# Performance work log

Measured on AMD Instinct MI355X. Metric: run time of the kernel, lower is better.

Reference implementation:

```python
import jax, jax.numpy as jnp
import numpy as np

DIM_Z = 256
N_HEADS = 8
R = DIM_Z // N_HEADS  # ternary_rank / rope head_dim
SCALE = 1.0           # ternary_scaling
THETA = 10000.0


def _rope_cos_sin(S, dtype):
    # returns cos, sin of shape [1, 1, S, R] (broadcast over batch and heads)
    inv_freq = 1.0 / (THETA ** (jnp.arange(0, R, 2, dtype=jnp.float32) / R))
    freqs = jnp.arange(S, dtype=jnp.float32)[:, None] * inv_freq[None, :]  # [S, R/2]
    emb = jnp.concatenate([freqs, freqs], axis=-1)  # [S, R]
    return jnp.cos(emb).astype(dtype)[None, None], jnp.sin(emb).astype(dtype)[None, None]


def _rot_half(x):
    h = x.shape[-1] // 2
    return jnp.concatenate([-x[..., h:], x[..., :h]], axis=-1)


def _apply(x, cos, sin):
    return x * cos + _rot_half(x) * sin


def _apply_o(x, cos, sin):
    return x * cos - _rot_half(x) * sin


def _compute_F(qz, mask, u, v, cos, sin):
    # qz: [N, S, D]; u, v: [D, D]; mask: [N, 1, S, S] or None
    N, S, D = qz.shape
    qu = (qz @ u.T) * SCALE
    qv = (qz @ v.T) * SCALE
    qu = qu.reshape(N, S, N_HEADS, R).transpose(0, 2, 1, 3)  # [N, H, S, R]
    qv = qv.reshape(N, S, N_HEADS, R).transpose(0, 2, 1, 3)
    qu_rot = _apply(qu, cos, sin)
    qu_o = _apply_o(qu, cos, sin)
    qv_rot = _apply(qv, cos, sin)
    F_mat = jnp.einsum('nhsr,nhtr->nhst', qu_rot, qv_rot)  # [N, H, S, S]
    if mask is not None:
        F_mat = F_mat + mask
    return F_mat, qu_o, qv_rot


def _compute_G(qh, qu_o, qv_rot, u, v, cos, sin):
    # qh: [N, H, S, S]
    N, H, S, _ = qh.shape
    g1 = _apply_o(jnp.einsum('nhst,nhtr->nhsr', qh, qv_rot), cos, sin)
    g2 = _apply(jnp.einsum('nhts,nhtr->nhsr', qh, qu_o), cos, sin)
    g1 = g1.transpose(0, 2, 1, 3).reshape(N, S, H * R)
    g2 = g2.transpose(0, 2, 1, 3).reshape(N, S, H * R)
    return (g1 @ u + g2 @ v) * SCALE  # [N, S, D]


def setup_inputs() -> dict:
    key = jax.random.key(0)
    ks = jax.random.split(key, 8)
    B, C, P, D = 8, 32, 128, DIM_Z
    std = 0.2  # ternary_init_std
    return {
        'qz': jax.random.normal(ks[0], (B, C, P, D), jnp.float32),
        'dep_mask_time': jax.random.normal(ks[1], (B * C, 1, P, P), jnp.float32),
        'dep_mask_chan': jax.random.normal(ks[2], (B * P, 1, C, C), jnp.float32),
        'u_time': std * jax.random.normal(ks[3], (D, D), jnp.float32),
        'v_time': std * jax.random.normal(ks[4], (D, D), jnp.float32),
        'u_chan': std * jax.random.normal(ks[5], (D, D), jnp.float32),
        'v_chan': std * jax.random.normal(ks[6], (D, D), jnp.float32),
    }


def reference(qz, dep_mask_time, dep_mask_chan, u_time, v_time, u_chan, v_chan):
    B, C, P, D = qz.shape
    H = N_HEADS
    cos_t, sin_t = _rope_cos_sin(P, qz.dtype)
    cos_c, sin_c = _rope_cos_sin(C, qz.dtype)

    qz_t = qz.reshape(B * C, P, D)
    F_t, quo_t, qv_t = _compute_F(qz_t, dep_mask_time, u_time, v_time, cos_t, sin_t)
    qz_c = qz.transpose(0, 2, 1, 3).reshape(B * P, C, D)
    F_c, quo_c, qv_c = _compute_F(qz_c, dep_mask_chan, u_chan, v_chan, cos_c, sin_c)

    # Joint softmax over combined time+channel candidates: [B, H, C, P, P+C]
    F_t_r = F_t.reshape(B, C, H, P, P).transpose(0, 2, 1, 3, 4)
    F_c_r = F_c.reshape(B, P, H, C, C).transpose(0, 2, 3, 1, 4)
    logits = jnp.concatenate([F_t_r, F_c_r], axis=-1)
    # regularize_h = 1/dim_z -> logits / regularize_h == logits * D; softmax in fp32
    qh = jax.nn.softmax(logits.astype(jnp.float32) * D, axis=-1)
    qh_t = qh[..., :P].transpose(0, 2, 1, 3, 4).reshape(B * C, H, P, P).astype(qz.dtype)
    qh_c = qh[..., P:].transpose(0, 3, 1, 2, 4).reshape(B * P, H, C, C).astype(qz.dtype)

    m_time = _compute_G(qh_t, quo_t, qv_t, u_time, v_time, cos_t, sin_t).reshape(B, C, P, D)
    m_chan = _compute_G(qh_c, quo_c, qv_c, u_chan, v_chan, cos_c, sin_c)
    m_chan = m_chan.reshape(B, P, C, D).transpose(0, 2, 1, 3)
    return m_time, m_chan
```

## Files before the change

### kernel.cpp

```cpp
#include <hip/hip_runtime.h>
#include <hip/hip_bf16.h>
#include <math.h>

#define LOG2T_16 0.8304820237218406f

typedef __attribute__((ext_vector_type(8))) short short8;
typedef __attribute__((ext_vector_type(4))) float f32x4;

#define PERM_LO 0x05040100u
#define PERM_HI 0x07060302u

__device__ __forceinline__ float bf2f(unsigned short u) {
    union { float f; unsigned int i; } x; x.i = ((unsigned int)u) << 16; return x.f;
}
__device__ __forceinline__ unsigned short f2b(float f) {
    __hip_bfloat16 h = __float2bfloat16(f);
    union { __hip_bfloat16 h; unsigned short u; } x; x.h = h; return x.u;
}

__device__ __forceinline__ float v5_dot32(const float* qurow, const float* row) {
    float dot = 0.f;
#pragma unroll
    for (int q = 0; q < 8; q++) {
        float4 x = *(const float4*)(row + q * 4);
        dot = fmaf(qurow[q * 4 + 0], x.x, dot);
        dot = fmaf(qurow[q * 4 + 1], x.y, dot);
        dot = fmaf(qurow[q * 4 + 2], x.z, dot);
        dot = fmaf(qurow[q * 4 + 3], x.w, dot);
    }
    return dot;
}

__device__ __forceinline__ void v5_fma32(float p_, const float* row, float* acc) {
#pragma unroll
    for (int q = 0; q < 8; q++) {
        float4 x = *(const float4*)(row + q * 4);
        float xs[4] = {x.x, x.y, x.z, x.w};
#pragma unroll
        for (int i = 0; i < 4; i++)
            acc[q * 4 + i] = fmaf(p_, xs[i], acc[q * 4 + i]);
    }
}

__global__ __launch_bounds__(256) void v10_prepB(
    const float* __restrict__ u_t, const float* __restrict__ v_t,
    const float* __restrict__ u_c, const float* __restrict__ v_c,
    unsigned int* __restrict__ Bp, unsigned int* __restrict__ Pp)
{
    __shared__ float Ts[64][65];
    const int mtx = blockIdx.y;
    const float* src = (mtx == 0) ? u_t : (mtx == 1) ? v_t : (mtx == 2) ? u_c : v_c;
    unsigned int* dst  = Bp + (size_t)mtx * 65536;
    unsigned int* pdst = Pp + (size_t)mtx * 65536;
    const int k0 = (blockIdx.x >> 2) * 64;
    const int c0 = (blockIdx.x & 3) * 64;
    const int tid = threadIdx.x;
    const int lr = tid >> 2;
    const int lc0 = (tid & 3) * 16;
    float av[16];
#pragma unroll
    for (int q = 0; q < 4; q++) {
        float4 x = *(const float4*)(src + (size_t)(k0 + lr) * 256 + c0 + lc0 + q * 4);
        *(float4*)&av[q * 4] = x;
        *(float4*)&Ts[lr][lc0 + q * 4] = x;
    }
#pragma unroll
    for (int q = 0; q < 4; q++) {
        unsigned int w[4];
#pragma unroll
        for (int e = 0; e < 4; e++) {
            float x = av[q * 4 + e];
            unsigned short hi = f2b(x);
            unsigned short lo = f2b(x - bf2f(hi));
            w[e] = (unsigned int)hi | ((unsigned int)lo << 16);
        }
        *(uint4*)(pdst + (size_t)(k0 + lr) * 256 + c0 + lc0 + q * 4) =
            make_uint4(w[0], w[1], w[2], w[3]);
    }
    __syncthreads();
#pragma unroll
    for (int q = 0; q < 4; q++) {
        unsigned int w[4];
#pragma unroll
        for (int e = 0; e < 4; e++) {
            float x = Ts[lc0 + q * 4 + e][lr];
            unsigned short hi = f2b(x);
            unsigned short lo = f2b(x - bf2f(hi));
            w[e] = (unsigned int)hi | ((unsigned int)lo << 16);
        }
        *(uint4*)(dst + (size_t)(c0 + lr) * 256 + k0 + lc0 + q * 4) =
            make_uint4(w[0], w[1], w[2], w[3]);
    }
}

__global__ __launch_bounds__(256) void v10_proj(
    const float* __restrict__ qz,
    const unsigned int* __restrict__ Pu, const unsigned int* __restrict__ Pv,
    float* __restrict__ qu_rot, float* __restrict__ qv_rot, int chan, int posmask)
{
    __shared__ __align__(16) unsigned short Ah[128][40];
    __shared__ __align__(16) unsigned short Al[128][40];
    __shared__ __align__(16) unsigned short Bh[128][40];
    __shared__ __align__(16) unsigned short Bl[128][40];
    const int row0 = blockIdx.x * 128;
    const int col0 = blockIdx.y * 128;
    const unsigned int* Bsrc = (col0 < 256) ? Pu : Pv;
    float* Cout = (col0 < 256) ? qu_rot : qv_rot;
    const int ccol0 = col0 & 255;
    const int tid = threadIdx.x;
    const int sr = tid >> 1;
    const int sk = (tid & 1) * 16;
    const int wv = tid >> 6;
    const int lane = tid & 63;
    const int wr = (wv >> 1) * 64, wc = (wv & 1) * 64;
    const int fr = lane & 15;
    const int fk = (lane >> 4) * 8;

    int arow = row0 + sr;
    if (chan) {
        int b = arow >> 12, p = (arow >> 5) & 127, c = arow & 31;
        arow = (b * 32 + c) * 128 + p;
    }
    const float* aptr = qz + (size_t)arow * 256 + sk;
    const unsigned int* bptr = Bsrc + (size_t)(ccol0 + sr) * 256 + sk;

    f32x4 acc[4][4] = {};

    for (int k0 = 0; k0 < 256; k0 += 32) {
        float av[16];
#pragma unroll
        for (int q = 0; q < 4; q++)
            *(float4*)&av[q * 4] = *(const float4*)(aptr + k0 + q * 4);
        unsigned int wh[8], wl[8];
#pragma unroll
        for (int e = 0; e < 8; e++) {
            unsigned short h0 = f2b(av[2 * e]), h1 = f2b(av[2 * e + 1]);
            unsigned short l0 = f2b(av[2 * e] - bf2f(h0));
            unsigned short l1 = f2b(av[2 * e + 1] - bf2f(h1));
            wh[e] = (unsigned int)h0 | ((unsigned int)h1 << 16);
            wl[e] = (unsigned int)l0 | ((unsigned int)l1 << 16);
        }
        *(uint4*)&Ah[sr][sk]     = make_uint4(wh[0], wh[1], wh[2], wh[3]);
        *(uint4*)&Ah[sr][sk + 8] = make_uint4(wh[4], wh[5], wh[6], wh[7]);
        *(uint4*)&Al[sr][sk]     = make_uint4(wl[0], wl[1], wl[2], wl[3]);
        *(uint4*)&Al[sr][sk + 8] = make_uint4(wl[4], wl[5], wl[6], wl[7]);
#pragma unroll
        for (int q = 0; q < 4; q++) {
            uint4 w = *(const uint4*)(bptr + k0 + q * 4);
            *(uint2*)&Bh[sr][sk + q * 4] = make_uint2(
                __builtin_amdgcn_perm(w.y, w.x, PERM_LO),
                __builtin_amdgcn_perm(w.w, w.z, PERM_LO));
            *(uint2*)&Bl[sr][sk + q * 4] = make_uint2(
                __builtin_amdgcn_perm(w.y, w.x, PERM_HI),
                __builtin_amdgcn_perm(w.w, w.z, PERM_HI));
        }
        __syncthreads();
        short8 ah[4], al[4];
#pragma unroll
        for (int i = 0; i < 4; i++) {
            ah[i] = *(const short8*)&Ah[wr + i * 16 + fr][fk];
            al[i] = *(const short8*)&Al[wr + i * 16 + fr][fk];
        }
#pragma unroll
        for (int j = 0; j < 4; j++) {
            const int bc = wc + j * 16 + fr;
            short8 bh = *(const short8*)&Bh[bc][fk];
            short8 bl = *(const short8*)&Bl[bc][fk];
#pragma unroll
            for (int i = 0; i < 4; i++) {
                acc[i][j] = __builtin_amdgcn_mfma_f32_16x16x32_bf16(ah[i], bh, acc[i][j], 0, 0, 0);
                acc[i][j] = __builtin_amdgcn_mfma_f32_16x16x32_bf16(ah[i], bl, acc[i][j], 0, 0, 0);
                acc[i][j] = __builtin_amdgcn_mfma_f32_16x16x32_bf16(al[i], bh, acc[i][j], 0, 0, 0);
                acc[i][j] = __builtin_amdgcn_mfma_f32_16x16x32_bf16(al[i], bl, acc[i][j], 0, 0, 0);
            }
        }
        __syncthreads();
    }
    const float fscale = exp2f(-(float)fr * LOG2T_16);
#pragma unroll
    for (int i = 0; i < 4; i++) {
#pragma unroll
        for (int r = 0; r < 4; r++) {
            int mr = row0 + wr + i * 16 + (lane >> 4) * 4 + r;
            float pos = (float)(mr & posmask);
            float sn, cs;
            sincosf(pos * fscale, &sn, &cs);
            float* op = Cout + (size_t)mr * 256 + ccol0 + wc + fr;
#pragma unroll
            for (int t = 0; t < 2; t++) {
                float x = acc[i][2 * t][r], y = acc[i][2 * t + 1][r];
                op[t * 32]      = x * cs - y * sn;
                op[t * 32 + 16] = y * cs + x * sn;
            }
        }
    }
}

__global__ __launch_bounds__(256) void v5_stats_t(
    const float* __restrict__ quR, const float* __restrict__ qvR,
    const float* __restrict__ mask, float* __restrict__ omax, float* __restrict__ osum)
{
    __shared__ float Qv[128][36];
    const int bid = blockIdx.x;
    const int n = bid & 255, h = bid >> 8;
    const int b = n >> 5, c = n & 31;
    const int tid = threadIdx.x;
    for (int idx = tid * 4; idx < 4096; idx += 1024) {
        int s = idx >> 5, r = idx & 31;
        *(float4*)&Qv[s][r] = *(const float4*)(qvR + ((size_t)(n * 128 + s)) * 256 + h * 32 + r);
    }
    const int s = tid >> 1, toff = (tid & 1) * 64;
    float qurow[32];
    const float* qptr = quR + ((size_t)(n * 128 + s)) * 256 + h * 32;
#pragma unroll
    for (int q = 0; q < 8; q++) {
        float4 x = *(const float4*)(qptr + q * 4);
        qurow[q * 4 + 0] = x.x; qurow[q * 4 + 1] = x.y; qurow[q * 4 + 2] = x.z; qurow[q * 4 + 3] = x.w;
    }
    __syncthreads();
    const float* mrow = mask + (size_t)n * 16384 + s * 128 + toff;
    float mx = -1e30f, sm = 0.f;
#pragma unroll 4
    for (int t = 0; t < 64; t++) {
        float dot = v5_dot32(qurow, &Qv[toff + t][0]);
        float vv = 256.f * (dot + mrow[t]);
        float nm = fmaxf(mx, vv);
        sm = sm * __expf(mx - nm) + __expf(vv - nm);
        mx = nm;
    }
    float omx = __shfl_xor(mx, 1);
    float osm = __shfl_xor(sm, 1);
    float fm = fmaxf(mx, omx);
    float fs = sm * __expf(mx - fm) + osm * __expf(omx - fm);
    if ((tid & 1) == 0) {
        int idx = ((b * 8 + h) * 32 + c) * 128 + s;
        omax[idx] = fm; osum[idx] = fs;
    }
}

__global__ __launch_bounds__(256) void v5_stats_c(
    const float* __restrict__ quR, const float* __restrict__ qvR,
    const float* __restrict__ mask, float* __restrict__ omax, float* __restrict__ osum)
{
    __shared__ float Qv[32][260];
    const int m = blockIdx.x;
    const int b = m >> 7, p = m & 127;
    const int tid = threadIdx.x;
    for (int idx = tid * 4; idx < 8192; idx += 1024) {
        int sc = idx >> 8, dd = idx & 255;
        *(float4*)&Qv[sc][dd] = *(const float4*)(qvR + ((size_t)m * 32 + sc) * 256 + dd);
    }
    const int h = tid >> 5, sc = tid & 31;
    float qurow[32];
    const float* qptr = quR + ((size_t)m * 32 + sc) * 256 + h * 32;
#pragma unroll
    for (int q = 0; q < 8; q++) {
        float4 x = *(const float4*)(qptr + q * 4);
        qurow[q * 4 + 0] = x.x; qurow[q * 4 + 1] = x.y; qurow[q * 4 + 2] = x.z; qurow[q * 4 + 3] = x.w;
    }
    __syncthreads();
    const float* mrow = mask + (size_t)m * 1024 + sc * 32;
    float mx = -1e30f, sm = 0.f;
#pragma unroll 4
    for (int t = 0; t < 32; t++) {
        float dot = v5_dot32(qurow, &Qv[t][h * 32]);
        float vv = 256.f * (dot + mrow[t]);
        float nm = fmaxf(mx, vv);
        sm = sm * __expf(mx - nm) + __expf(vv - nm);
        mx = nm;
    }
    int idx = ((b * 8 + h) * 32 + sc) * 128 + p;
    omax[idx] = mx; osum[idx] = sm;
}

__global__ __launch_bounds__(256) void v5_merge(
    const float* __restrict__ mt, const float* __restrict__ st,
    const float* __restrict__ mc, const float* __restrict__ sc,
    float* __restrict__ Mo, float* __restrict__ So)
{
    int i = blockIdx.x * 256 + threadIdx.x;
    float a = mt[i], b = mc[i];
    float mx = fmaxf(a, b);
    float s = st[i] * __expf(a - mx) + sc[i] * __expf(b - mx);
    Mo[i] = mx;
    So[i] = 1.f / s;
}

__global__ __launch_bounds__(256) void v8_G_t(
    const float* quR, const float* qvR,
    const float* __restrict__ mask, const float* __restrict__ Mr, const float* __restrict__ Sv,
    unsigned short* gpl)
{
    __shared__ __align__(16) unsigned short Pm[16384];
    __shared__ __align__(16) float Qv[128][36];
    unsigned short* QT = (unsigned short*)&Qv[0][0];
    const int bid = blockIdx.x;
    const int n = bid & 255, h = bid >> 8;
    const int b = n >> 5, c = n & 31;
    const int tid = threadIdx.x;
    const int lane = tid & 63, wv = tid >> 6;
    const int fr = lane & 15, kgl = lane >> 4;

    for (int idx = tid * 4; idx < 4096; idx += 1024) {
        int s = idx >> 5, r = idx & 31;
        *(float4*)&Qv[s][r] = *(const float4*)(qvR + ((size_t)(n * 128 + s)) * 256 + h * 32 + r);
    }
    {
        const int s = tid >> 1, toff = (tid & 1) * 64;
        float qurow[32];
        const float* qptr = quR + ((size_t)(n * 128 + s)) * 256 + h * 32;
#pragma unroll
        for (int q = 0; q < 8; q++) {
            float4 x = *(const float4*)(qptr + q * 4);
            qurow[q * 4 + 0] = x.x; qurow[q * 4 + 1] = x.y; qurow[q * 4 + 2] = x.z; qurow[q * 4 + 3] = x.w;
        }
        __syncthreads();
        const int rowidx = ((b * 8 + h) * 32 + c) * 128 + s;
        const float Mx = Mr[rowidx];
        const float Si = Sv[rowidx];
        const float* mrow = mask + (size_t)n * 16384 + s * 128 + toff;
#pragma unroll 4
        for (int t = 0; t < 64; t++) {
            float dot = v5_dot32(qurow, &Qv[toff + t][0]);
            float pv = __expf(256.f * (dot + mrow[t]) - Mx) * Si;
            int tg = toff + t;
            int ct = (((tg >> 3) ^ (s & 15)) << 3) | (tg & 7);
            Pm[s * 128 + ct] = f2b(pv);
        }
    }
    __syncthreads();
    {
        const int t = tid >> 1, rh = (tid & 1) * 16;
        const float* src = qvR + ((size_t)(n * 128 + t)) * 256 + h * 32 + rh;
        float v[16];
#pragma unroll
        for (int q = 0; q < 4; q++)
            *(float4*)&v[q * 4] = *(const float4*)(src + q * 4);
#pragma unroll
        for (int i = 0; i < 16; i++) {
            int r = rh + i;
            unsigned short hi = f2b(v[i]);
            unsigned short lo = f2b(v[i] - bf2f(hi));
            int ct = (((t >> 3) ^ (r & 15)) << 3) | (t & 7);
            QT[r * 128 + ct] = hi;
            QT[4096 + r * 128 + ct] = lo;
        }
    }
    __syncthreads();
    unsigned int g1h[8];
    {
        f32x4 acc[2][2] = {};
#pragma unroll
        for (int kw = 0; kw < 4; kw++) {
            short8 a[2];
#pragma unroll
            for (int i = 0; i < 2; i++) {
                int row = wv * 32 + i * 16 + fr;
                a[i] = *(const short8*)&Pm[row * 128 + (((kw * 4 + kgl) ^ (row & 15)) << 3)];
            }
            short8 bh[2], bl[2];
#pragma unroll
            for (int j = 0; j < 2; j++) {
                int r = j * 16 + fr;
                int off = r * 128 + (((kw * 4 + kgl) ^ (r & 15)) << 3);
                bh[j] = *(const short8*)&QT[off];
                bl[j] = *(const short8*)&QT[4096 + off];
            }
#pragma unroll
            for (int i = 0; i < 2; i++)
#pragma unroll
                for (int j = 0; j < 2; j++) {
                    acc[i][j] = __builtin_amdgcn_mfma_f32_16x16x32_bf16(a[i], bh[j], acc[i][j], 0, 0, 0);
                    acc[i][j] = __builtin_amdgcn_mfma_f32_16x16x32_bf16(a[i], bl[j], acc[i][j], 0, 0, 0);
                }
        }
#pragma unroll
        for (int i = 0; i < 2; i++)
#pragma unroll
            for (int reg = 0; reg < 4; reg++) {
                int s = wv * 32 + i * 16 + kgl * 4 + reg;
                float ang = (float)s * exp2f(-(float)fr * LOG2T_16);
                float sn, cs;
                __sincosf(ang, &sn, &cs);
                float x = acc[i][0][reg], y = acc[i][1][reg];
                g1h[i * 4 + reg] = (unsigned int)f2b(x * cs + y * sn)
                                 | ((unsigned int)f2b(y * cs - x * sn) << 16);
            }
    }
    __syncthreads();
    {
        const int t = tid >> 1, jh = (tid & 1) * 8;
        const float* base = quR + ((size_t)(n * 128 + t)) * 256 + h * 32;
        float aa[8], bb[8];
        *(float4*)&aa[0] = *(const float4*)(base + jh);
        *(float4*)&aa[4] = *(const float4*)(base + jh + 4);
        *(float4*)&bb[0] = *(const float4*)(base + jh + 16);
        *(float4*)&bb[4] = *(const float4*)(base + jh + 20);
#pragma unroll
        for (int i = 0; i < 8; i++) {
            int j = jh + i;
            float ang = 2.f * (float)t * exp2f(-(float)j * LOG2T_16);
            float s2, c2;
            __sincosf(ang, &s2, &c2);
            float o1 = aa[i] * c2 + bb[i] * s2;
            float o2 = bb[i] * c2 - aa[i] * s2;
            int ct1 = (((t >> 3) ^ (j & 15)) << 3) | (t & 7);
            unsigned short h1 = f2b(o1);
            QT[j * 128 + ct1] = h1;
            QT[4096 + j * 128 + ct1] = f2b(o1 - bf2f(h1));
            int r2 = j + 16;
            int ct2 = (((t >> 3) ^ (r2 & 15)) << 3) | (t & 7);
            unsigned short h2 = f2b(o2);
            QT[r2 * 128 + ct2] = h2;
            QT[4096 + r2 * 128 + ct2] = f2b(o2 - bf2f(h2));
        }
    }
    __syncthreads();
    unsigned int g2h[8];
    {
        f32x4 acc[2][2] = {};
#pragma unroll
        for (int kw = 0; kw < 4; kw++) {
            short8 ah[2], al[2];
#pragma unroll
            for (int i = 0; i < 2; i++) {
                int r = i * 16 + fr;
                int off = r * 128 + (((kw * 4 + kgl) ^ (r & 15)) << 3);
                ah[i] = *(const short8*)&QT[off];
                al[i] = *(const short8*)&QT[4096 + off];
            }
            short8 bfr[2];
#pragma unroll
            for (int jj = 0; jj < 2; jj++) {
                int scol = (2 * wv + jj) * 16 + fr;
#pragma unroll
                for (int j = 0; j < 8; j++) {
                    int t = kw * 32 + kgl * 8 + j;
                    int ct = (((scol >> 3) ^ (t & 15)) << 3) | (scol & 7);
                    bfr[jj][j] = (short)Pm[t * 128 + ct];
                }
            }
#pragma unroll
            for (int i = 0; i < 2; i++)
#pragma unroll
                for (int jj = 0; jj < 2; jj++) {
                    acc[i][jj] = __builtin_amdgcn_mfma_f32_16x16x32_bf16(ah[i], bfr[jj], acc[i][jj], 0, 0, 0);
                    acc[i][jj] = __builtin_amdgcn_mfma_f32_16x16x32_bf16(al[i], bfr[jj], acc[i][jj], 0, 0, 0);
                }
        }
#pragma unroll
        for (int jj = 0; jj < 2; jj++)
#pragma unroll
            for (int reg = 0; reg < 4; reg++) {
                int sv = (2 * wv + jj) * 16 + fr;
                int r = kgl * 4 + reg;
                float ang = (float)sv * exp2f(-(float)r * LOG2T_16);
                float sn, cs;
                __sincosf(ang, &sn, &cs);
                float x = acc[0][jj][reg], y = acc[1][jj][reg];
                g2h[jj * 4 + reg] = (unsigned int)f2b(x * cs - y * sn)
                                  | ((unsigned int)f2b(y * cs + x * sn) << 16);
            }
    }
    __syncthreads();
    {
#pragma unroll
        for (int i = 0; i < 2; i++)
#pragma unroll
            for (int reg = 0; reg < 4; reg++) {
                int s = wv * 32 + i * 16 + kgl * 4 + reg;
                unsigned int w = g1h[i * 4 + reg];
                Pm[s * 32 + fr] = (unsigned short)w;
                Pm[s * 32 + fr + 16] = (unsigned short)(w >> 16);
            }
#pragma unroll
        for (int jj = 0; jj < 2; jj++)
#pragma unroll
            for (int reg = 0; reg < 4; reg++) {
                int s = (2 * wv + jj) * 16 + fr;
                int r = kgl * 4 + reg;
                unsigned int w = g2h[jj * 4 + reg];
                Pm[4096 + s * 32 + r] = (unsigned short)w;
                Pm[4096 + s * 32 + r + 16] = (unsigned short)(w >> 16);
            }
    }
    __syncthreads();
    {
        const int s = tid >> 1, rh = (tid & 1) * 16;
        size_t baseu = ((size_t)(n * 128 + s)) * 512 + h * 64 + rh;
        *(uint4*)(gpl + baseu)      = *(const uint4*)&Pm[s * 32 + rh];
        *(uint4*)(gpl + baseu + 8)  = *(const uint4*)&Pm[s * 32 + rh + 8];
        *(uint4*)(gpl + baseu + 32) = *(const uint4*)&Pm[4096 + s * 32 + rh];
        *(uint4*)(gpl + baseu + 40) = *(const uint4*)&Pm[4096 + s * 32 + rh + 8];
    }
}

__global__ __launch_bounds__(256) void v8_G_c(
    const float* quR, const float* qvR,
    const float* __restrict__ mask, const float* __restrict__ Mr, const float* __restrict__ Sv,
    unsigned short* gpl)
{
    __shared__ float Qv[32][260];
    __shared__ unsigned short Pm[8][32][34];
    const int m = blockIdx.x;
    const int b = m >> 7, p = m & 127;
    const int tid = threadIdx.x;
    for (int idx = tid * 4; idx < 8192; idx += 1024) {
        int sc = idx >> 8, dd = idx & 255;
        *(float4*)&Qv[sc][dd] = *(const float4*)(qvR + ((size_t)m * 32 + sc) * 256 + dd);
    }
    const int h = tid >> 5, sc = tid & 31;
    {
        float qurow[32];
        const float* qptr = quR + ((size_t)m * 32 + sc) * 256 + h * 32;
#pragma unroll
        for (int q = 0; q < 8; q++) {
            float4 x = *(const float4*)(qptr + q * 4);
            qurow[q * 4 + 0] = x.x; qurow[q * 4 + 1] = x.y; qurow[q * 4 + 2] = x.z; qurow[q * 4 + 3] = x.w;
        }
        __syncthreads();
        const int rowidx = ((b * 8 + h) * 32 + sc) * 128 + p;
        const float Mx = Mr[rowidx], Si = Sv[rowidx];
        const float* mrow = mask + (size_t)m * 1024 + sc * 32;
#pragma unroll 4
        for (int t = 0; t < 32; t++) {
            float dot = v5_dot32(qurow, &Qv[t][h * 32]);
            float pv = __expf(256.f * (dot + mrow[t]) - Mx) * Si;
            Pm[h][t][sc] = f2b(pv);
        }
    }
    __syncthreads();
    float a[32] = {};
#pragma unroll 4
    for (int t = 0; t < 32; t++) {
        float p_ = bf2f(Pm[h][t][sc]);
        v5_fma32(p_, &Qv[t][h * 32], a);
    }
    float cs[16], sn[16];
#pragma unroll
    for (int i = 0; i < 16; i++) {
        float ang = (float)sc * exp2f(-(float)i * LOG2T_16);
        __sincosf(ang, &sn[i], &cs[i]);
    }
    unsigned int g1p[8], g1q[8];
#pragma unroll
    for (int j = 0; j < 8; j++) {
        int i0 = 2 * j, i1 = 2 * j + 1;
        float x0 = a[i0], y0 = a[16 + i0], x1 = a[i1], y1 = a[16 + i1];
        g1p[j] = (unsigned int)f2b(x0 * cs[i0] + y0 * sn[i0])
               | ((unsigned int)f2b(x1 * cs[i1] + y1 * sn[i1]) << 16);
        g1q[j] = (unsigned int)f2b(y0 * cs[i0] - x0 * sn[i0])
               | ((unsigned int)f2b(y1 * cs[i1] - x1 * sn[i1]) << 16);
    }
    __syncthreads();
    for (int idx = tid * 4; idx < 4096; idx += 1024) {
        int row = idx >> 7, rem = idx & 127;
        int h2 = rem >> 4, j0 = rem & 15;
        const float* base = quR + ((size_t)m * 32 + row) * 256 + h2 * 32;
        float4 a4 = *(const float4*)(base + j0);
        float4 b4 = *(const float4*)(base + j0 + 16);
        float aa[4] = {a4.x, a4.y, a4.z, a4.w};
        float bb[4] = {b4.x, b4.y, b4.z, b4.w};
        float o1[4], o2[4];
#pragma unroll
        for (int i = 0; i < 4; i++) {
            float ang = 2.f * (float)row * exp2f(-(float)(j0 + i) * LOG2T_16);
            float s2, c2;
            __sincosf(ang, &s2, &c2);
            o1[i] = aa[i] * c2 + bb[i] * s2;
            o2[i] = bb[i] * c2 - aa[i] * s2;
        }
        *(float4*)&Qv[row][h2 * 32 + j0]      = make_float4(o1[0], o1[1], o1[2], o1[3]);
        *(float4*)&Qv[row][h2 * 32 + j0 + 16] = make_float4(o2[0], o2[1], o2[2], o2[3]);
    }
    __syncthreads();
#pragma unroll
    for (int i = 0; i < 32; i++) a[i] = 0.f;
#pragma unroll 4
    for (int t = 0; t < 32; t++) {
        float p_ = bf2f(Pm[h][sc][t]);
        v5_fma32(p_, &Qv[t][h * 32], a);
    }
    unsigned int* gpu = (unsigned int*)gpl;
    size_t ub = ((size_t)m * 32 + sc) * 256 + h * 32;
    *(uint4*)(gpu + ub)      = make_uint4(g1p[0], g1p[1], g1p[2], g1p[3]);
    *(uint4*)(gpu + ub + 4)  = make_uint4(g1p[4], g1p[5], g1p[6], g1p[7]);
    *(uint4*)(gpu + ub + 8)  = make_uint4(g1q[0], g1q[1], g1q[2], g1q[3]);
    *(uint4*)(gpu + ub + 12) = make_uint4(g1q[4], g1q[5], g1q[6], g1q[7]);
    unsigned int p2[8], q2[8];
#pragma unroll
    for (int j = 0; j < 8; j++) {
        int i0 = 2 * j, i1 = 2 * j + 1;
        p2[j] = (unsigned int)f2b(a[i0] * cs[i0] - a[16 + i0] * sn[i0])
              | ((unsigned int)f2b(a[i1] * cs[i1] - a[16 + i1] * sn[i1]) << 16);
        q2[j] = (unsigned int)f2b(a[16 + i0] * cs[i0] + a[i0] * sn[i0])
              | ((unsigned int)f2b(a[16 + i1] * cs[i1] + a[i1] * sn[i1]) << 16);
    }
    *(uint4*)(gpu + ub + 16) = make_uint4(p2[0], p2[1], p2[2], p2[3]);
    *(uint4*)(gpu + ub + 20) = make_uint4(p2[4], p2[5], p2[6], p2[7]);
    *(uint4*)(gpu + ub + 24) = make_uint4(q2[0], q2[1], q2[2], q2[3]);
    *(uint4*)(gpu + ub + 28) = make_uint4(q2[4], q2[5], q2[6], q2[7]);
}

__global__ __launch_bounds__(256) void v8_outgemm(
    const unsigned short* __restrict__ gpl,
    const unsigned int* __restrict__ Bu,
    const unsigned int* __restrict__ Bv,
    float* __restrict__ out, int remap)
{
    __shared__ __align__(16) unsigned short A1[128][40];
    __shared__ __align__(16) unsigned short A2[128][40];
    __shared__ __align__(16) unsigned short Bh[2][128][40];
    __shared__ __align__(16) unsigned short Bl[2][128][40];
    const int row0 = blockIdx.x * 128;
    const int col0 = blockIdx.y * 128;
    const int tid = threadIdx.x;
    const int sr = tid >> 1;
    const int sk = (tid & 1) * 16;
    const int wv = tid >> 6;
    const int lane = tid & 63;
    const int wr = (wv >> 1) * 64, wc = (wv & 1) * 64;
    const int fr = lane & 15;
    const int fk = (lane >> 4) * 8;

    const unsigned int* uptr = Bu + (size_t)(col0 + sr) * 256 + sk;
    const unsigned int* vptr = Bv + (size_t)(col0 + sr) * 256 + sk;

    f32x4 acc[4][4] = {};

    for (int k0 = 0; k0 < 256; k0 += 32) {
        int kb = k0 + sk;
        const unsigned short* ap = gpl + (size_t)(row0 + sr) * 512 + ((kb >> 5) << 6) + (kb & 31);
        *(uint4*)&A1[sr][sk]     = *(const uint4*)ap;
        *(uint4*)&A1[sr][sk + 8] = *(const uint4*)(ap + 8);
        *(uint4*)&A2[sr][sk]     = *(const uint4*)(ap + 32);
        *(uint4*)&A2[sr][sk + 8] = *(const uint4*)(ap + 40);
#pragma unroll
        for (int q = 0; q < 4; q++) {
            uint4 wU = *(const uint4*)(uptr + k0 + q * 4);
            *(uint2*)&Bh[0][sr][sk + q * 4] = make_uint2(
                __builtin_amdgcn_perm(wU.y, wU.x, PERM_LO),
                __builtin_amdgcn_perm(wU.w, wU.z, PERM_LO));
            *(uint2*)&Bl[0][sr][sk + q * 4] = make_uint2(
                __builtin_amdgcn_perm(wU.y, wU.x, PERM_HI),
                __builtin_amdgcn_perm(wU.w, wU.z, PERM_HI));
            uint4 wV = *(const uint4*)(vptr + k0 + q * 4);
            *(uint2*)&Bh[1][sr][sk + q * 4] = make_uint2(
                __builtin_amdgcn_perm(wV.y, wV.x, PERM_LO),
                __builtin_amdgcn_perm(wV.w, wV.z, PERM_LO));
            *(uint2*)&Bl[1][sr][sk + q * 4] = make_uint2(
                __builtin_amdgcn_perm(wV.y, wV.x, PERM_HI),
                __builtin_amdgcn_perm(wV.w, wV.z, PERM_HI));
        }
        __syncthreads();
        short8 a1[4], a2[4];
#pragma unroll
        for (int i = 0; i < 4; i++) {
            a1[i] = *(const short8*)&A1[wr + i * 16 + fr][fk];
            a2[i] = *(const short8*)&A2[wr + i * 16 + fr][fk];
        }
#pragma unroll
        for (int j = 0; j < 4; j++) {
            const int bc = wc + j * 16 + fr;
            short8 buh = *(const short8*)&Bh[0][bc][fk];
            short8 bul = *(const short8*)&Bl[0][bc][fk];
            short8 bvh = *(const short8*)&Bh[1][bc][fk];
            short8 bvl = *(const short8*)&Bl[1][bc][fk];
#pragma unroll
            for (int i = 0; i < 4; i++) {
                acc[i][j] = __builtin_amdgcn_mfma_f32_16x16x32_bf16(a1[i], buh, acc[i][j], 0, 0, 0);
                acc[i][j] = __builtin_amdgcn_mfma_f32_16x16x32_bf16(a1[i], bul, acc[i][j], 0, 0, 0);
                acc[i][j] = __builtin_amdgcn_mfma_f32_16x16x32_bf16(a2[i], bvh, acc[i][j], 0, 0, 0);
                acc[i][j] = __builtin_amdgcn_mfma_f32_16x16x32_bf16(a2[i], bvl, acc[i][j], 0, 0, 0);
            }
        }
        __syncthreads();
    }
#pragma unroll
    for (int i = 0; i < 4; i++) {
#pragma unroll
        for (int r = 0; r < 4; r++) {
            int mr = row0 + wr + i * 16 + (lane >> 4) * 4 + r;
            int orow = mr;
            if (remap) {
                int bb = mr >> 12, pp = (mr >> 5) & 127, cc = mr & 31;
                orow = (bb << 12) + (cc << 7) + pp;
            }
            float* op = out + (size_t)orow * 256 + col0 + wc + fr;
#pragma unroll
            for (int j = 0; j < 4; j++)
                op[j * 16] = acc[i][j][r];
        }
    }
}

extern "C" void kernel_launch(void* const* d_in, const int* in_sizes, int n_in,
                              void* d_out, int out_size, void* d_ws, size_t ws_size,
                              hipStream_t stream)
{
    (void)in_sizes; (void)n_in; (void)out_size; (void)ws_size;
    const float* qz     = (const float*)d_in[0];
    const float* mask_t = (const float*)d_in[1];
    const float* mask_c = (const float*)d_in[2];
    const float* u_time = (const float*)d_in[3];
    const float* v_time = (const float*)d_in[4];
    const float* u_chan = (const float*)d_in[5];
    const float* v_chan = (const float*)d_in[6];
    float* out = (float*)d_out;
    float* W = (float*)d_ws;

    float* quR_t = W;
    float* qvR_t = W + 8388608;
    float* quR_c = W + 16777216;
    float* qvR_c = W + 25165824;
    float* S     = W + 33554432;
    float* max_t = S;
    float* sum_t = S + 262144;
    float* max_c = S + 524288;
    float* sum_c = S + 786432;
    float* Mrow  = S + 1048576;
    float* Sinv  = S + 1310720;
    unsigned int* BP = (unsigned int*)(W + 35127296);
    unsigned int* PP = BP + 262144;
    unsigned short* GPt = (unsigned short*)quR_t;
    unsigned short* GPc = (unsigned short*)quR_c;

    dim3 blk(256);
    v10_prepB<<<dim3(16, 4), blk, 0, stream>>>(u_time, v_time, u_chan, v_chan, BP, PP);
    v10_proj<<<dim3(256, 4), blk, 0, stream>>>(qz, PP, PP + 65536, quR_t, qvR_t, 0, 127);
    v10_proj<<<dim3(256, 4), blk, 0, stream>>>(qz, PP + 131072, PP + 196608, quR_c, qvR_c, 1, 31);
    v5_stats_t<<<2048, blk, 0, stream>>>(quR_t, qvR_t, mask_t, max_t, sum_t);
    v5_stats_c<<<1024, blk, 0, stream>>>(quR_c, qvR_c, mask_c, max_c, sum_c);
    v5_merge<<<1024, blk, 0, stream>>>(max_t, sum_t, max_c, sum_c, Mrow, Sinv);
    v8_G_t<<<2048, blk, 0, stream>>>(quR_t, qvR_t, mask_t, Mrow, Sinv, GPt);
    v8_outgemm<<<dim3(256, 2), blk, 0, stream>>>(GPt, BP, BP + 65536, out, 0);
    v8_G_c<<<1024, blk, 0, stream>>>(quR_c, qvR_c, mask_c, Mrow, Sinv, GPc);
    v8_outgemm<<<dim3(256, 2), blk, 0, stream>>>(GPc, BP + 131072, BP + 196608, out + 8388608, 1);
}
```

Measured before the change: 526.2 us.

## Compute time-axis QK logits with split-bf16 MFMA in stats and G kernels

Replaces the scalar fp32 dot-product loops that compute the time-axis F logits, in both the softmax-statistics kernel and the G_t kernel, with MFMA tiles. Inputs are split into bf16 hi/lo pairs and combined with four MFMAs to keep close to fp32 accuracy. Row max and sum are reduced across lanes with shuffles and across waves through shared memory. The goal is to remove the VALU-bound QK^T work, at the cost of extra split conversions, more LDS traffic and a scattered, column-strided mask read pattern.

Measured after the change: 444.9 us. 1.18x faster.

```diff
diff --git a/kernel.cpp b/kernel.cpp
--- a/kernel.cpp
+++ b/kernel.cpp
@@ -39,6 +39,62 @@
 #pragma unroll
         for (int i = 0; i < 4; i++)
             acc[q * 4 + i] = fmaf(p_, xs[i], acc[q * 4 + i]);
+    }
+}
+
+__device__ __forceinline__ void qk_stage_splits(
+    const float* __restrict__ quR, const float* __restrict__ qvR,
+    int n, int h, int tid,
+    unsigned short* QUh, unsigned short* QUl,
+    unsigned short* QVh, unsigned short* QVl)
+{
+    for (int idx = tid * 4; idx < 4096; idx += 1024) {
+        int s = idx >> 5, r = idx & 31;
+        size_t go = ((size_t)(n * 128 + s)) * 256 + h * 32 + r;
+        float4 xu = *(const float4*)(quR + go);
+        float4 xv = *(const float4*)(qvR + go);
+        float us[4] = {xu.x, xu.y, xu.z, xu.w};
+        float vs[4] = {xv.x, xv.y, xv.z, xv.w};
+        unsigned short uh[4], ul[4], vh[4], vl[4];
+#pragma unroll
+        for (int e = 0; e < 4; e++) {
+            uh[e] = f2b(us[e]); ul[e] = f2b(us[e] - bf2f(uh[e]));
+            vh[e] = f2b(vs[e]); vl[e] = f2b(vs[e] - bf2f(vh[e]));
+        }
+        int lo = s * 40 + r;
+        *(uint2*)&QUh[lo] = make_uint2((unsigned)uh[0] | ((unsigned)uh[1] << 16),
+                                       (unsigned)uh[2] | ((unsigned)uh[3] << 16));
+        *(uint2*)&QUl[lo] = make_uint2((unsigned)ul[0] | ((unsigned)ul[1] << 16),
+                                       (unsigned)ul[2] | ((unsigned)ul[3] << 16));
+        *(uint2*)&QVh[lo] = make_uint2((unsigned)vh[0] | ((unsigned)vh[1] << 16),
+                                       (unsigned)vh[2] | ((unsigned)vh[3] << 16));
+        *(uint2*)&QVl[lo] = make_uint2((unsigned)vl[0] | ((unsigned)vl[1] << 16),
+                                       (unsigned)vl[2] | ((unsigned)vl[3] << 16));
+    }
+}
+
+__device__ __forceinline__ void qk_mfma(
+    const unsigned short* QUh, const unsigned short* QUl,
+    const unsigned short* QVh, const unsigned short* QVl,
+    int wr, int wc, int fr, int fk, f32x4 acc[4][4])
+{
+    short8 ah[4], al[4];
+#pragma unroll
+    for (int i = 0; i < 4; i++) {
+        ah[i] = *(const short8*)&QUh[(wr + i * 16 + fr) * 40 + fk];
+        al[i] = *(const short8*)&QUl[(wr + i * 16 + fr) * 40 + fk];
+    }
+#pragma unroll
+    for (int j = 0; j < 4; j++) {
+        short8 bh = *(const short8*)&QVh[(wc + j * 16 + fr) * 40 + fk];
+        short8 bl = *(const short8*)&QVl[(wc + j * 16 + fr) * 40 + fk];
+#pragma unroll
+        for (int i = 0; i < 4; i++) {
+            acc[i][j] = __builtin_amdgcn_mfma_f32_16x16x32_bf16(al[i], bl, acc[i][j], 0, 0, 0);
+            acc[i][j] = __builtin_amdgcn_mfma_f32_16x16x32_bf16(al[i], bh, acc[i][j], 0, 0, 0);
+            acc[i][j] = __builtin_amdgcn_mfma_f32_16x16x32_bf16(ah[i], bl, acc[i][j], 0, 0, 0);
+            acc[i][j] = __builtin_amdgcn_mfma_f32_16x16x32_bf16(ah[i], bh, acc[i][j], 0, 0, 0);
+        }
     }
 }
 
@@ -196,45 +252,70 @@
     }
 }
 
-__global__ __launch_bounds__(256) void v5_stats_t(
+__global__ __launch_bounds__(256) void v11_stats_t(
     const float* __restrict__ quR, const float* __restrict__ qvR,
     const float* __restrict__ mask, float* __restrict__ omax, float* __restrict__ osum)
 {
-    __shared__ float Qv[128][36];
+    __shared__ __align__(16) unsigned short QUh[5120];
+    __shared__ __align__(16) unsigned short QUl[5120];
+    __shared__ __align__(16) unsigned short QVh[5120];
+    __shared__ __align__(16) unsigned short QVl[5120];
+    __shared__ float Mp[128][2];
+    __shared__ float Sp[128][2];
     const int bid = blockIdx.x;
     const int n = bid & 255, h = bid >> 8;
     const int b = n >> 5, c = n & 31;
     const int tid = threadIdx.x;
-    for (int idx = tid * 4; idx < 4096; idx += 1024) {
-        int s = idx >> 5, r = idx & 31;
-        *(float4*)&Qv[s][r] = *(const float4*)(qvR + ((size_t)(n * 128 + s)) * 256 + h * 32 + r);
-    }
-    const int s = tid >> 1, toff = (tid & 1) * 64;
-    float qurow[32];
-    const float* qptr = quR + ((size_t)(n * 128 + s)) * 256 + h * 32;
-#pragma unroll
-    for (int q = 0; q < 8; q++) {
-        float4 x = *(const float4*)(qptr + q * 4);
-        qurow[q * 4 + 0] = x.x; qurow[q * 4 + 1] = x.y; qurow[q * 4 + 2] = x.z; qurow[q * 4 + 3] = x.w;
-    }
-    __syncthreads();
-    const float* mrow = mask + (size_t)n * 16384 + s * 128 + toff;
-    float mx = -1e30f, sm = 0.f;
-#pragma unroll 4
-    for (int t = 0; t < 64; t++) {
-        float dot = v5_dot32(qurow, &Qv[toff + t][0]);
-        float vv = 256.f * (dot + mrow[t]);
-        float nm = fmaxf(mx, vv);
-        sm = sm * __expf(mx - nm) + __expf(vv - nm);
-        mx = nm;
-    }
-    float omx = __shfl_xor(mx, 1);
-    float osm = __shfl_xor(sm, 1);
-    float fm = fmaxf(mx, omx);
-    float fs = sm * __expf(mx - fm) + osm * __expf(omx - fm);
-    if ((tid & 1) == 0) {
+    const int lane = tid & 63, wv = tid >> 6;
+    const int wr = (wv >> 1) * 64, wc = (wv & 1) * 64;
+    const int fr = lane & 15, fk = (lane >> 4) * 8;
+
+    qk_stage_splits(quR, qvR, n, h, tid, QUh, QUl, QVh, QVl);
+    __syncthreads();
+    f32x4 acc[4][4] = {};
+    qk_mfma(QUh, QUl, QVh, QVl, wr, wc, fr, fk, acc);
+    const float* mbase = mask + (size_t)n * 16384;
+#pragma unroll
+    for (int i = 0; i < 4; i++)
+#pragma unroll
+        for (int j = 0; j < 4; j++) {
+            int t = wc + j * 16 + fr;
+#pragma unroll
+            for (int reg = 0; reg < 4; reg++) {
+                int s = wr + i * 16 + (lane >> 4) * 4 + reg;
+                acc[i][j][reg] = 256.f * (acc[i][j][reg] + mbase[s * 128 + t]);
+            }
+        }
+#pragma unroll
+    for (int i = 0; i < 4; i++)
+#pragma unroll
+        for (int reg = 0; reg < 4; reg++) {
+            float m = fmaxf(fmaxf(acc[i][0][reg], acc[i][1][reg]),
+                            fmaxf(acc[i][2][reg], acc[i][3][reg]));
+            m = fmaxf(m, __shfl_xor(m, 1));
+            m = fmaxf(m, __shfl_xor(m, 2));
+            m = fmaxf(m, __shfl_xor(m, 4));
+            m = fmaxf(m, __shfl_xor(m, 8));
+            float sm = __expf(acc[i][0][reg] - m) + __expf(acc[i][1][reg] - m)
+                     + __expf(acc[i][2][reg] - m) + __expf(acc[i][3][reg] - m);
+            sm += __shfl_xor(sm, 1);
+            sm += __shfl_xor(sm, 2);
+            sm += __shfl_xor(sm, 4);
+            sm += __shfl_xor(sm, 8);
+            if (fr == 0) {
+                int s = wr + i * 16 + (lane >> 4) * 4 + reg;
+                Mp[s][wc >> 6] = m;
+                Sp[s][wc >> 6] = sm;
+            }
+        }
+    __syncthreads();
+    if (tid < 128) {
+        int s = tid;
+        float m0 = Mp[s][0], m1 = Mp[s][1];
+        float M = fmaxf(m0, m1);
+        float S = Sp[s][0] * __expf(m0 - M) + Sp[s][1] * __expf(m1 - M);
         int idx = ((b * 8 + h) * 32 + c) * 128 + s;
-        omax[idx] = fm; osum[idx] = fs;
+        omax[idx] = M; osum[idx] = S;
     }
 }
 
@@ -286,46 +367,56 @@
     So[i] = 1.f / s;
 }
 
-__global__ __launch_bounds__(256) void v8_G_t(
+__global__ __launch_bounds__(256) void v11_G_t(
     const float* quR, const float* qvR,
     const float* __restrict__ mask, const float* __restrict__ Mr, const float* __restrict__ Sv,
     unsigned short* gpl)
 {
-    __shared__ __align__(16) unsigned short Pm[16384];
-    __shared__ __align__(16) float Qv[128][36];
-    unsigned short* QT = (unsigned short*)&Qv[0][0];
+    __shared__ __align__(16) unsigned char LB[49152];
+    unsigned short* Pm  = (unsigned short*)LB;
+    unsigned short* QT  = (unsigned short*)(LB + 32768);
+    unsigned short* QUh = (unsigned short*)LB;
+    unsigned short* QUl = QUh + 5120;
+    unsigned short* QVh = QUh + 10240;
+    unsigned short* QVl = QUh + 15360;
     const int bid = blockIdx.x;
     const int n = bid & 255, h = bid >> 8;
     const int b = n >> 5, c = n & 31;
     const int tid = threadIdx.x;
     const int lane = tid & 63, wv = tid >> 6;
+    const int wr = (wv >> 1) * 64, wc = (wv & 1) * 64;
     const int fr = lane & 15, kgl = lane >> 4;
-
-    for (int idx = tid * 4; idx < 4096; idx += 1024) {
-        int s = idx >> 5, r = idx & 31;
-        *(float4*)&Qv[s][r] = *(const float4*)(qvR + ((size_t)(n * 128 + s)) * 256 + h * 32 + r);
-    }
+    const int fk = kgl * 8;
+
+    qk_stage_splits(quR, qvR, n, h, tid, QUh, QUl, QVh, QVl);
+    __syncthreads();
     {
-        const int s = tid >> 1, toff = (tid & 1) * 64;
-        float qurow[32];
-        const float* qptr = quR + ((size_t)(n * 128 + s)) * 256 + h * 32;
-#pragma unroll
-        for (int q = 0; q < 8; q++) {
-            float4 x = *(const float4*)(qptr + q * 4);
-            qurow[q * 4 + 0] = x.x; qurow[q * 4 + 1] = x.y; qurow[q * 4 + 2] = x.z; qurow[q * 4 + 3] = x.w;
-        }
+        f32x4 acc[4][4] = {};
+        qk_mfma(QUh, QUl, QVh, QVl, wr, wc, fr, fk, acc);
         __syncthreads();
-        const int rowidx = ((b * 8 + h) * 32 + c) * 128 + s;
-        const float Mx = Mr[rowidx];
-        const float Si = Sv[rowidx];
-        const float* mrow = mask + (size_t)n * 16384 + s * 128 + toff;
-#pragma unroll 4
-        for (int t = 0; t < 64; t++) {
-            float dot = v5_dot32(qurow, &Qv[toff + t][0]);
-            float pv = __expf(256.f * (dot + mrow[t]) - Mx) * Si;
-            int tg = toff + t;
-            int ct = (((tg >> 3) ^ (s & 15)) << 3) | (tg & 7);
-            Pm[s * 128 + ct] = f2b(pv);
+        const float* mbase = mask + (size_t)n * 16384;
+        const int rowbase = ((b * 8 + h) * 32 + c) * 128;
+#pragma unroll
+        for (int i = 0; i < 4; i++) {
+            float Mx4[4], Si4[4];
+#pragma unroll
+            for (int reg = 0; reg < 4; reg++) {
+                int s = wr + i * 16 + kgl * 4 + reg;
+                Mx4[reg] = Mr[rowbase + s];
+                Si4[reg] = Sv[rowbase + s];
+            }
+#pragma unroll
+            for (int j = 0; j < 4; j++) {
+                int t = wc + j * 16 + fr;
+#pragma unroll
+                for (int reg = 0; reg < 4; reg++) {
+                    int s = wr + i * 16 + kgl * 4 + reg;
+                    float vv = 256.f * (acc[i][j][reg] + mbase[s * 128 + t]);
+                    float pv = __expf(vv - Mx4[reg]) * Si4[reg];
+                    int ct = (((t >> 3) ^ (s & 15)) << 3) | (t & 7);
+                    Pm[s * 128 + ct] = f2b(pv);
+                }
+            }
         }
     }
     __syncthreads();
@@ -729,10 +820,10 @@
     v10_prepB<<<dim3(16, 4), blk, 0, stream>>>(u_time, v_time, u_chan, v_chan, BP, PP);
     v10_proj<<<dim3(256, 4), blk, 0, stream>>>(qz, PP, PP + 65536, quR_t, qvR_t, 0, 127);
     v10_proj<<<dim3(256, 4), blk, 0, stream>>>(qz, PP + 131072, PP + 196608, quR_c, qvR_c, 1, 31);
-    v5_stats_t<<<2048, blk, 0, stream>>>(quR_t, qvR_t, mask_t, max_t, sum_t);
+    v11_stats_t<<<2048, blk, 0, stream>>>(quR_t, qvR_t, mask_t, max_t, sum_t);
     v5_stats_c<<<1024, blk, 0, stream>>>(quR_c, qvR_c, mask_c, max_c, sum_c);
     v5_merge<<<1024, blk, 0, stream>>>(max_t, sum_t, max_c, sum_c, Mrow, Sinv);
-    v8_G_t<<<2048, blk, 0, stream>>>(quR_t, qvR_t, mask_t, Mrow, Sinv, GPt);
+    v11_G_t<<<2048, blk, 0, stream>>>(quR_t, qvR_t, mask_t, Mrow, Sinv, GPt);
     v8_outgemm<<<dim3(256, 2), blk, 0, stream>>>(GPt, BP, BP + 65536, out, 0);
     v8_G_c<<<1024, blk, 0, stream>>>(quR_c, qvR_c, mask_c, Mrow, Sinv, GPc);
     v8_outgemm<<<dim3(256, 2), blk, 0, stream>>>(GPc, BP + 131072, BP + 196608, out + 8388608, 1);
```
